# Performance work log

Hardware: AMD Instinct MI355X
Metric: run time of the kernel (lower is better)

Reference implementation:

```python
import jax, jax.numpy as jnp
import numpy as np

B, N, F_IN, F_OUT = 64, 4096, 32, 32


def setup_inputs() -> dict:
    key = jax.random.key(0)
    k1, k2, k3, k4 = jax.random.split(key, 4)
    x = jax.random.normal(k1, (B, N, F_IN), dtype=jnp.float32)
    adj = jax.random.uniform(k2, (N, N), dtype=jnp.float32)
    # GraphConvolution parameters (Glorot-ish scale)
    W = jax.random.normal(k3, (F_IN, F_OUT), dtype=jnp.float32) / np.sqrt(F_IN)
    b = jax.random.normal(k4, (F_OUT,), dtype=jnp.float32) * 0.01
    return {"x": x, "adj": adj, "W": W, "b": b}


def reference(x, adj, W, b):
    # Original: adj_ = kron(I_B, adj) -> block-diagonal [B*N, B*N];
    # gconv(x_flat, adj_) = adj_ @ (x_flat @ W) + b, reshaped to [B, N, F_OUT].
    # Block-diagonal structure == independent per-batch graph conv:
    #   out[b] = adj @ (x[b] @ W) + b
    support = jnp.einsum('bnf,fo->bno', x, W)      # [B, N, F_OUT]
    out = jnp.einsum('nm,bmo->bno', adj, support)  # [B, N, F_OUT]
    return out + b
```

## Files before the change

### kernel.cpp

```cpp
#include <hip/hip_runtime.h>
#include <hip/hip_bf16.h>


#define B_SZ 64
#define N_SZ 4096
#define NT 64

typedef __attribute__((ext_vector_type(8))) short bf16x8;
typedef __attribute__((ext_vector_type(4))) float f32x4;
typedef __attribute__((ext_vector_type(8))) unsigned short u16x8;

__device__ __forceinline__ unsigned short f2bf(float f) {
  unsigned int u = __float_as_uint(f);
  u += 0x7fffu + ((u >> 16) & 1u);
  return (unsigned short)(u >> 16);
}

__device__ __forceinline__ void support_body(const float* __restrict__ x,
                                             const float* __restrict__ W,
                                             unsigned short* __restrict__ St,
                                             int gid) {
  const int m = gid & (N_SZ - 1);
  const int b = gid >> 12;
  const float4* xr = (const float4*)(x + (size_t)gid * 32);
  float xv[32];
#pragma unroll
  for (int i = 0; i < 8; ++i) {
    float4 v = xr[i];
    xv[4 * i + 0] = v.x; xv[4 * i + 1] = v.y;
    xv[4 * i + 2] = v.z; xv[4 * i + 3] = v.w;
  }
  const size_t obase = ((size_t)b * 32) * (size_t)N_SZ + m;
#pragma unroll
  for (int o = 0; o < 32; ++o) {
    float acc = 0.f;
#pragma unroll
    for (int f = 0; f < 32; ++f) acc = fmaf(xv[f], W[f * 32 + o], acc);
    St[obase + (size_t)o * N_SZ] = f2bf(acc);
  }
}

__device__ __forceinline__ void cvt_body(const float* __restrict__ a,
                                         unsigned short* __restrict__ o,
                                         size_t idx8) {
  const size_t i = idx8 * 8;
  const float4* p = (const float4*)(a + i);
  float4 v0 = p[0], v1 = p[1];
  u16x8 r;
  r[0] = f2bf(v0.x); r[1] = f2bf(v0.y); r[2] = f2bf(v0.z); r[3] = f2bf(v0.w);
  r[4] = f2bf(v1.x); r[5] = f2bf(v1.y); r[6] = f2bf(v1.z); r[7] = f2bf(v1.w);
  *(u16x8*)(o + i) = r;
}

__global__ __launch_bounds__(256) void k_prep(const float* __restrict__ x,
                                              const float* __restrict__ adj,
                                              const float* __restrict__ W,
                                              unsigned short* __restrict__ St,
                                              unsigned short* __restrict__ adjB) {
  const int bid = blockIdx.x;
  const int t = threadIdx.x;
  if (bid < 8192) cvt_body(adj, adjB, (size_t)bid * 256 + t);
  else support_body(x, W, St, (bid - 8192) * 256 + t);
}

__global__ __launch_bounds__(256) void k_support(const float* __restrict__ x,
                                                 const float* __restrict__ W,
                                                 unsigned short* __restrict__ St) {
  support_body(x, W, St, blockIdx.x * 256 + threadIdx.x);
}
__global__ __launch_bounds__(256) void k_cvt(const float* __restrict__ a,
                                             unsigned short* __restrict__ o) {
  cvt_body(a, o, (size_t)blockIdx.x * 256 + threadIdx.x);
}

#define GLOAD16(gp, lp)                                                        \
  __builtin_amdgcn_global_load_lds(                                            \
      (const __attribute__((address_space(1))) void*)(gp),                     \
      (__attribute__((address_space(3))) void*)(lp), 16, 0, 0)
#define PRIO1() __builtin_amdgcn_s_setprio(1)
#define PRIO0() __builtin_amdgcn_s_setprio(0)

__global__ __launch_bounds__(256, 2) void k_gemm6(const unsigned short* __restrict__ Ab,
                                                  const unsigned short* __restrict__ Bm,
                                                  const float* __restrict__ bias,
                                                  float* __restrict__ out,
                                                  int nbm, int rowoff) {
  __shared__ __attribute__((aligned(16))) char SM[65536];
  char* Lc = SM;
  char* Lo = SM + 32768;
  const int t = threadIdx.x;
  const int wg = blockIdx.x;
  const int xcd = wg & 7;
  const int c = wg >> 3;
  const int bm0 = (xcd * nbm + (c >> 4)) << 7;
  const int bn0 = (c & 15) << 7;
  const int lane = t & 63;
  const int wid = t >> 6;
  const int wr = wid & 1;
  const int ks = wid >> 1;

  f32x4 acc[4][8];
#pragma unroll
  for (int i = 0; i < 4; ++i)
#pragma unroll
    for (int j = 0; j < 8; ++j) acc[i][j] = (f32x4){0.f, 0.f, 0.f, 0.f};

  const int srow = t >> 3;
  const int as = t & 7;
  const int swz = (as ^ (srow & 7)) << 4;
  const size_t a_s0 = ((size_t)(bm0 + srow) << 13) + (size_t)swz;
  const size_t b_s0 = ((size_t)(bn0 + srow) << 13) + (size_t)swz;
  const int t16 = t * 16;
  const char* A8 = (const char*)Ab;
  const char* B8 = (const char*)Bm;

#define STAGE(KT_, Ld)                                                         \
  do {                                                                         \
    const size_t kb = (size_t)(KT_) << 7;                                      \
    GLOAD16(A8 + a_s0 + kb,          (Ld) + t16);                              \
    GLOAD16(A8 + a_s0 + 262144 + kb, (Ld) + 4096 + t16);                       \
    GLOAD16(A8 + a_s0 + 524288 + kb, (Ld) + 8192 + t16);                       \
    GLOAD16(A8 + a_s0 + 786432 + kb, (Ld) + 12288 + t16);                      \
    GLOAD16(B8 + b_s0 + kb,          (Ld) + 16384 + t16);                      \
    GLOAD16(B8 + b_s0 + 262144 + kb, (Ld) + 20480 + t16);                      \
    GLOAD16(B8 + b_s0 + 524288 + kb, (Ld) + 24576 + t16);                      \
    GLOAD16(B8 + b_s0 + 786432 + kb, (Ld) + 28672 + t16);                      \
  } while (0)

  const int cbase = (ks * 64 + ((lane >> 4) << 4)) ^ ((lane & 7) << 4);
  int aoff[4], boff[8];
#pragma unroll
  for (int mi = 0; mi < 4; ++mi)
    aoff[mi] = (wr * 64 + mi * 16 + (lane & 15)) * 128 + cbase;
#pragma unroll
  for (int ni = 0; ni < 8; ++ni)
    boff[ni] = 16384 + (ni * 16 + (lane & 15)) * 128 + cbase;

  STAGE(0, Lc);
  __syncthreads();

  for (int kt = 0; kt < NT; ++kt) {
    if (kt + 1 < NT) STAGE(kt + 1, Lo);
    bf16x8 a[4], b[8];
#pragma unroll
    for (int mi = 0; mi < 4; ++mi) a[mi] = *(const bf16x8*)(Lc + aoff[mi]);
#pragma unroll
    for (int ni = 0; ni < 8; ++ni) b[ni] = *(const bf16x8*)(Lc + boff[ni]);
    PRIO1();
#pragma unroll
    for (int mi = 0; mi < 4; ++mi)
#pragma unroll
      for (int ni = 0; ni < 8; ++ni)
        acc[mi][ni] = __builtin_amdgcn_mfma_f32_16x16x32_bf16(
            a[mi], b[ni], acc[mi][ni], 0, 0, 0);
    PRIO0();
    __syncthreads();
    { char* tp_ = Lc; Lc = Lo; Lo = tp_; }
  }

  if (ks == 1) {
    char* mb = SM + (wr << 15);
#pragma unroll
    for (int mi = 0; mi < 4; ++mi)
#pragma unroll
      for (int ni = 0; ni < 8; ++ni)
        *(f32x4*)(mb + (((mi * 8 + ni) << 6) + lane) * 16) = acc[mi][ni];
  }
  __syncthreads();
  if (ks == 0) {
    char* mb = SM + (wr << 15);
#pragma unroll
    for (int mi = 0; mi < 4; ++mi)
#pragma unroll
      for (int ni = 0; ni < 8; ++ni)
        acc[mi][ni] += *(const f32x4*)(mb + (((mi * 8 + ni) << 6) + lane) * 16);
    const float blo = bias[lane & 15];
    const float bhi = bias[(lane & 15) + 16];
#pragma unroll
    for (int mi = 0; mi < 4; ++mi) {
#pragma unroll
      for (int ni = 0; ni < 8; ++ni) {
        const float badd = (ni & 1) ? bhi : blo;
#pragma unroll
        for (int q = 0; q < 4; ++q) {
          const int n = rowoff + bm0 + wr * 64 + mi * 16 + ((lane >> 4) << 2) + q;
          const int cidx = bn0 + ni * 16 + (lane & 15);
          const int bb = cidx >> 5;
          const int o = cidx & 31;
          out[(((size_t)bb << 12) + n) * 32 + o] = acc[mi][ni][q] + badd;
        }
      }
    }
  }
}

extern "C" void kernel_launch(void* const* d_in, const int* in_sizes, int n_in,
                              void* d_out, int out_size, void* d_ws, size_t ws_size,
                              hipStream_t stream) {
  const float* x = (const float*)d_in[0];
  const float* adj = (const float*)d_in[1];
  const float* W = (const float*)d_in[2];
  const float* bias = (const float*)d_in[3];
  float* out = (float*)d_out;

  const size_t ST_B = (size_t)2048 * 4096 * 2;
  const size_t ADJ_FULL = (size_t)4096 * 4096 * 2;

  unsigned short* St = (unsigned short*)d_ws;

  if (ws_size >= ST_B + ADJ_FULL) {
    unsigned short* adjB = St + (ST_B / 2);
    hipLaunchKernelGGL(k_prep, dim3(9216), dim3(256), 0, stream, x, adj, W, St,
                       adjB);
    hipLaunchKernelGGL(k_gemm6, dim3(512), dim3(256), 0, stream, adjB, St, bias,
                       out, 4, 0);
  } else {
    unsigned short* adjH = St + (ST_B / 2);
    hipLaunchKernelGGL(k_support, dim3((B_SZ * N_SZ) / 256), dim3(256), 0,
                       stream, x, W, St);
    hipLaunchKernelGGL(k_cvt, dim3((2048 * 4096) / 2048), dim3(256), 0, stream,
                       adj, adjH);
    hipLaunchKernelGGL(k_gemm6, dim3(256), dim3(256), 0, stream, adjH, St, bias,
                       out, 2, 0);
    hipLaunchKernelGGL(k_cvt, dim3((2048 * 4096) / 2048), dim3(256), 0, stream,
                       adj + (size_t)2048 * 4096, adjH);
    hipLaunchKernelGGL(k_gemm6, dim3(256), dim3(256), 0, stream, adjH, St, bias,
                       out, 2, 2048);
  }
}
```

Measured before the change: 94.20 us.

## Widen GEMM tile to 128x256 with 512 threads and triple-buffered LDS pipeline

Replaces the 128x128 double-buffered GEMM with a 128x256 tile computed by 8 waves: two column halves, each split over two K halves. A three-stage LDS ring is prefetched two iterations ahead, with explicit vmcnt waits and raw barriers in place of __syncthreads. The intent is to raise A-tile reuse, halve the workgroup count and hide global load latency better. In exchange the kernel uses 144KB of LDS per block, so only one block fits per CU despite the launch bound hint, and the hand-placed waitcnt and barrier scheme is fragile.

```diff
diff --git a/kernel.cpp b/kernel.cpp
--- a/kernel.cpp
+++ b/kernel.cpp
@@ -5,6 +5,7 @@
 #define B_SZ 64
 #define N_SZ 4096
 #define NT 64
+#define STG 49152
 
 typedef __attribute__((ext_vector_type(8))) short bf16x8;
 typedef __attribute__((ext_vector_type(4))) float f32x4;
@@ -79,25 +80,28 @@
       (__attribute__((address_space(3))) void*)(lp), 16, 0, 0)
 #define PRIO1() __builtin_amdgcn_s_setprio(1)
 #define PRIO0() __builtin_amdgcn_s_setprio(0)
-
-__global__ __launch_bounds__(256, 2) void k_gemm6(const unsigned short* __restrict__ Ab,
+#define VMW(N_) asm volatile("s_waitcnt vmcnt(" #N_ ")" ::: "memory")
+#define LGKM0() asm volatile("s_waitcnt lgkmcnt(0)" ::: "memory")
+#define BARR() asm volatile("s_barrier" ::: "memory")
+#define SCHED0() __builtin_amdgcn_sched_barrier(0)
+
+__global__ __launch_bounds__(512, 2) void k_gemm8(const unsigned short* __restrict__ Ab,
                                                   const unsigned short* __restrict__ Bm,
                                                   const float* __restrict__ bias,
                                                   float* __restrict__ out,
                                                   int nbm, int rowoff) {
-  __shared__ __attribute__((aligned(16))) char SM[65536];
-  char* Lc = SM;
-  char* Lo = SM + 32768;
+  __shared__ __attribute__((aligned(16))) char SM[147456];
   const int t = threadIdx.x;
   const int wg = blockIdx.x;
   const int xcd = wg & 7;
   const int c = wg >> 3;
-  const int bm0 = (xcd * nbm + (c >> 4)) << 7;
-  const int bn0 = (c & 15) << 7;
+  const int bm0 = (xcd * nbm + (c >> 3)) << 7;
+  const int bn0 = (c & 7) << 8;
   const int lane = t & 63;
   const int wid = t >> 6;
   const int wr = wid & 1;
-  const int ks = wid >> 1;
+  const int nc = (wid >> 1) & 1;
+  const int ks = wid >> 2;
 
   f32x4 acc[4][8];
 #pragma unroll
@@ -114,17 +118,15 @@
   const char* A8 = (const char*)Ab;
   const char* B8 = (const char*)Bm;
 
-#define STAGE(KT_, Ld)                                                         \
+#define STAGE(KT_, LOFF_)                                                      \
   do {                                                                         \
     const size_t kb = (size_t)(KT_) << 7;                                      \
-    GLOAD16(A8 + a_s0 + kb,          (Ld) + t16);                              \
-    GLOAD16(A8 + a_s0 + 262144 + kb, (Ld) + 4096 + t16);                       \
-    GLOAD16(A8 + a_s0 + 524288 + kb, (Ld) + 8192 + t16);                       \
-    GLOAD16(A8 + a_s0 + 786432 + kb, (Ld) + 12288 + t16);                      \
-    GLOAD16(B8 + b_s0 + kb,          (Ld) + 16384 + t16);                      \
-    GLOAD16(B8 + b_s0 + 262144 + kb, (Ld) + 20480 + t16);                      \
-    GLOAD16(B8 + b_s0 + 524288 + kb, (Ld) + 24576 + t16);                      \
-    GLOAD16(B8 + b_s0 + 786432 + kb, (Ld) + 28672 + t16);                      \
+    GLOAD16(A8 + a_s0 + kb,           SM + (LOFF_) + t16);                     \
+    GLOAD16(A8 + a_s0 + 524288 + kb,  SM + (LOFF_) + 8192 + t16);              \
+    GLOAD16(B8 + b_s0 + kb,           SM + (LOFF_) + 16384 + t16);             \
+    GLOAD16(B8 + b_s0 + 524288 + kb,  SM + (LOFF_) + 24576 + t16);             \
+    GLOAD16(B8 + b_s0 + 1048576 + kb, SM + (LOFF_) + 32768 + t16);             \
+    GLOAD16(B8 + b_s0 + 1572864 + kb, SM + (LOFF_) + 40960 + t16);             \
   } while (0)
 
   const int cbase = (ks * 64 + ((lane >> 4) << 4)) ^ ((lane & 7) << 4);
@@ -134,32 +136,53 @@
     aoff[mi] = (wr * 64 + mi * 16 + (lane & 15)) * 128 + cbase;
 #pragma unroll
   for (int ni = 0; ni < 8; ++ni)
-    boff[ni] = 16384 + (ni * 16 + (lane & 15)) * 128 + cbase;
-
-  STAGE(0, Lc);
-  __syncthreads();
-
-  for (int kt = 0; kt < NT; ++kt) {
-    if (kt + 1 < NT) STAGE(kt + 1, Lo);
-    bf16x8 a[4], b[8];
-#pragma unroll
-    for (int mi = 0; mi < 4; ++mi) a[mi] = *(const bf16x8*)(Lc + aoff[mi]);
-#pragma unroll
-    for (int ni = 0; ni < 8; ++ni) b[ni] = *(const bf16x8*)(Lc + boff[ni]);
-    PRIO1();
-#pragma unroll
-    for (int mi = 0; mi < 4; ++mi)
-#pragma unroll
-      for (int ni = 0; ni < 8; ++ni)
-        acc[mi][ni] = __builtin_amdgcn_mfma_f32_16x16x32_bf16(
-            a[mi], b[ni], acc[mi][ni], 0, 0, 0);
-    PRIO0();
-    __syncthreads();
-    { char* tp_ = Lc; Lc = Lo; Lo = tp_; }
-  }
+    boff[ni] = 16384 + (nc * 128 + ni * 16 + (lane & 15)) * 128 + cbase;
+
+#define FRAG_MFMA(CUROFF_)                                                     \
+  do {                                                                         \
+    bf16x8 a[4], b[8];                                                         \
+    _Pragma("unroll") for (int mi = 0; mi < 4; ++mi)                           \
+        a[mi] = *(const bf16x8*)(SM + (CUROFF_) + aoff[mi]);                   \
+    _Pragma("unroll") for (int ni = 0; ni < 8; ++ni)                           \
+        b[ni] = *(const bf16x8*)(SM + (CUROFF_) + boff[ni]);                   \
+    LGKM0();                                                                   \
+    SCHED0();                                                                  \
+    BARR();                                                                    \
+    PRIO1();                                                                   \
+    _Pragma("unroll") for (int mi = 0; mi < 4; ++mi)                           \
+        _Pragma("unroll") for (int ni = 0; ni < 8; ++ni)                       \
+            acc[mi][ni] = __builtin_amdgcn_mfma_f32_16x16x32_bf16(             \
+                a[mi], b[ni], acc[mi][ni], 0, 0, 0);                           \
+    PRIO0();                                                                   \
+  } while (0)
+
+#define ITER(T_, CUR_, NXT_)                                                   \
+  do {                                                                         \
+    STAGE((T_) + 2, (NXT_) * STG);                                             \
+    VMW(12);                                                                   \
+    BARR();                                                                    \
+    FRAG_MFMA((CUR_) * STG);                                                   \
+  } while (0)
+
+  STAGE(0, 0);
+  STAGE(1, STG);
+
+  for (int t0 = 0; t0 < 60; t0 += 3) {
+    ITER(t0 + 0, 0, 2);
+    ITER(t0 + 1, 1, 0);
+    ITER(t0 + 2, 2, 1);
+  }
+  ITER(60, 0, 2);
+  ITER(61, 1, 0);
+  VMW(6);
+  BARR();
+  FRAG_MFMA(2 * STG);
+  VMW(0);
+  BARR();
+  FRAG_MFMA(0 * STG);
 
   if (ks == 1) {
-    char* mb = SM + (wr << 15);
+    char* mb = SM + ((wid & 3) << 15);
 #pragma unroll
     for (int mi = 0; mi < 4; ++mi)
 #pragma unroll
@@ -168,7 +191,7 @@
   }
   __syncthreads();
   if (ks == 0) {
-    char* mb = SM + (wr << 15);
+    char* mb = SM + ((wid & 3) << 15);
 #pragma unroll
     for (int mi = 0; mi < 4; ++mi)
 #pragma unroll
@@ -184,7 +207,7 @@
 #pragma unroll
         for (int q = 0; q < 4; ++q) {
           const int n = rowoff + bm0 + wr * 64 + mi * 16 + ((lane >> 4) << 2) + q;
-          const int cidx = bn0 + ni * 16 + (lane & 15);
+          const int cidx = bn0 + nc * 128 + ni * 16 + (lane & 15);
           const int bb = cidx >> 5;
           const int o = cidx & 31;
           out[(((size_t)bb << 12) + n) * 32 + o] = acc[mi][ni][q] + badd;
@@ -212,7 +235,7 @@
     unsigned short* adjB = St + (ST_B / 2);
     hipLaunchKernelGGL(k_prep, dim3(9216), dim3(256), 0, stream, x, adj, W, St,
                        adjB);
-    hipLaunchKernelGGL(k_gemm6, dim3(512), dim3(256), 0, stream, adjB, St, bias,
+    hipLaunchKernelGGL(k_gemm8, dim3(256), dim3(512), 0, stream, adjB, St, bias,
                        out, 4, 0);
   } else {
     unsigned short* adjH = St + (ST_B / 2);
@@ -220,11 +243,11 @@
                        stream, x, W, St);
     hipLaunchKernelGGL(k_cvt, dim3((2048 * 4096) / 2048), dim3(256), 0, stream,
                        adj, adjH);
-    hipLaunchKernelGGL(k_gemm6, dim3(256), dim3(256), 0, stream, adjH, St, bias,
+    hipLaunchKernelGGL(k_gemm8, dim3(128), dim3(512), 0, stream, adjH, St, bias,
                        out, 2, 0);
     hipLaunchKernelGGL(k_cvt, dim3((2048 * 4096) / 2048), dim3(256), 0, stream,
                        adj + (size_t)2048 * 4096, adjH);
-    hipLaunchKernelGGL(k_gemm6, dim3(256), dim3(256), 0, stream, adjH, St, bias,
+    hipLaunchKernelGGL(k_gemm8, dim3(128), dim3(512), 0, stream, adjH, St, bias,
                        out, 2, 2048);
   }
 }
```

Result: slower. 96.89 us (+2.9%).

## Fuse fp32-to-bf16 adjacency conversion into GEMM A-tile loading

Applied to the files above, without the earlier changes.

The separate pass that converts the 4096x4096 adjacency matrix to bf16 in workspace is removed. The GEMM now reads fp32 adj rows straight into registers, converts them in-kernel and writes them to swizzled LDS, overlapping that store with the MFMA loop. This drops a 64MB read plus 32MB write-and-reread of adj. In exchange the GEMM moves twice the A-tile bytes per tile from global memory, uses more registers, and ALU work competes with the MFMAs. The tile-to-XCD mapping is also changed to 2D blocks of 1024x1024.

```diff
diff --git a/kernel.cpp b/kernel.cpp
--- a/kernel.cpp
+++ b/kernel.cpp
@@ -16,10 +16,10 @@
   return (unsigned short)(u >> 16);
 }
 
-__device__ __forceinline__ void support_body(const float* __restrict__ x,
-                                             const float* __restrict__ W,
-                                             unsigned short* __restrict__ St,
-                                             int gid) {
+__global__ __launch_bounds__(256) void k_support(const float* __restrict__ x,
+                                                 const float* __restrict__ W,
+                                                 unsigned short* __restrict__ St) {
+  const int gid = blockIdx.x * 256 + threadIdx.x;
   const int m = gid & (N_SZ - 1);
   const int b = gid >> 12;
   const float4* xr = (const float4*)(x + (size_t)gid * 32);
@@ -38,39 +38,6 @@
     for (int f = 0; f < 32; ++f) acc = fmaf(xv[f], W[f * 32 + o], acc);
     St[obase + (size_t)o * N_SZ] = f2bf(acc);
   }
-}
-
-__device__ __forceinline__ void cvt_body(const float* __restrict__ a,
-                                         unsigned short* __restrict__ o,
-                                         size_t idx8) {
-  const size_t i = idx8 * 8;
-  const float4* p = (const float4*)(a + i);
-  float4 v0 = p[0], v1 = p[1];
-  u16x8 r;
-  r[0] = f2bf(v0.x); r[1] = f2bf(v0.y); r[2] = f2bf(v0.z); r[3] = f2bf(v0.w);
-  r[4] = f2bf(v1.x); r[5] = f2bf(v1.y); r[6] = f2bf(v1.z); r[7] = f2bf(v1.w);
-  *(u16x8*)(o + i) = r;
-}
-
-__global__ __launch_bounds__(256) void k_prep(const float* __restrict__ x,
-                                              const float* __restrict__ adj,
-                                              const float* __restrict__ W,
-                                              unsigned short* __restrict__ St,
-                                              unsigned short* __restrict__ adjB) {
-  const int bid = blockIdx.x;
-  const int t = threadIdx.x;
-  if (bid < 8192) cvt_body(adj, adjB, (size_t)bid * 256 + t);
-  else support_body(x, W, St, (bid - 8192) * 256 + t);
-}
-
-__global__ __launch_bounds__(256) void k_support(const float* __restrict__ x,
-                                                 const float* __restrict__ W,
-                                                 unsigned short* __restrict__ St) {
-  support_body(x, W, St, blockIdx.x * 256 + threadIdx.x);
-}
-__global__ __launch_bounds__(256) void k_cvt(const float* __restrict__ a,
-                                             unsigned short* __restrict__ o) {
-  cvt_body(a, o, (size_t)blockIdx.x * 256 + threadIdx.x);
 }
 
 #define GLOAD16(gp, lp)                                                        \
@@ -80,20 +47,19 @@
 #define PRIO1() __builtin_amdgcn_s_setprio(1)
 #define PRIO0() __builtin_amdgcn_s_setprio(0)
 
-__global__ __launch_bounds__(256, 2) void k_gemm6(const unsigned short* __restrict__ Ab,
+__global__ __launch_bounds__(256, 2) void k_gemm7(const float* __restrict__ adj,
                                                   const unsigned short* __restrict__ Bm,
                                                   const float* __restrict__ bias,
-                                                  float* __restrict__ out,
-                                                  int nbm, int rowoff) {
+                                                  float* __restrict__ out) {
   __shared__ __attribute__((aligned(16))) char SM[65536];
   char* Lc = SM;
   char* Lo = SM + 32768;
   const int t = threadIdx.x;
   const int wg = blockIdx.x;
   const int xcd = wg & 7;
-  const int c = wg >> 3;
-  const int bm0 = (xcd * nbm + (c >> 4)) << 7;
-  const int bn0 = (c & 15) << 7;
+  const int idx = wg >> 3;
+  const int bm0 = ((xcd >> 1) << 10) + ((idx >> 3) << 7);
+  const int bn0 = ((xcd & 1) << 10) + ((idx & 7) << 7);
   const int lane = t & 63;
   const int wid = t >> 6;
   const int wr = wid & 1;
@@ -108,25 +74,43 @@
   const int srow = t >> 3;
   const int as = t & 7;
   const int swz = (as ^ (srow & 7)) << 4;
-  const size_t a_s0 = ((size_t)(bm0 + srow) << 13) + (size_t)swz;
   const size_t b_s0 = ((size_t)(bn0 + srow) << 13) + (size_t)swz;
   const int t16 = t * 16;
-  const char* A8 = (const char*)Ab;
   const char* B8 = (const char*)Bm;
 
-#define STAGE(KT_, Ld)                                                         \
+#define STAGE_B(KT_, Ld)                                                       \
   do {                                                                         \
     const size_t kb = (size_t)(KT_) << 7;                                      \
-    GLOAD16(A8 + a_s0 + kb,          (Ld) + t16);                              \
-    GLOAD16(A8 + a_s0 + 262144 + kb, (Ld) + 4096 + t16);                       \
-    GLOAD16(A8 + a_s0 + 524288 + kb, (Ld) + 8192 + t16);                       \
-    GLOAD16(A8 + a_s0 + 786432 + kb, (Ld) + 12288 + t16);                      \
     GLOAD16(B8 + b_s0 + kb,          (Ld) + 16384 + t16);                      \
     GLOAD16(B8 + b_s0 + 262144 + kb, (Ld) + 20480 + t16);                      \
     GLOAD16(B8 + b_s0 + 524288 + kb, (Ld) + 24576 + t16);                      \
     GLOAD16(B8 + b_s0 + 786432 + kb, (Ld) + 28672 + t16);                      \
   } while (0)
 
+  const float* aF = adj + ((size_t)(bm0 + (t >> 3)) << 12) + ((t & 7) << 3);
+  const int awbase = ((t >> 3) << 7) + (((t & 7) ^ ((t >> 3) & 7)) << 4);
+
+#define ALOAD(KT_)                                                             \
+  do {                                                                         \
+    const float* ap_ = aF + ((size_t)(KT_) << 6);                              \
+    _Pragma("unroll") for (int j = 0; j < 4; ++j) {                            \
+      va[2 * j]     = *(const float4*)(ap_ + (size_t)j * 131072);              \
+      va[2 * j + 1] = *(const float4*)(ap_ + (size_t)j * 131072 + 4);          \
+    }                                                                          \
+  } while (0)
+
+#define AWRITE(Ld)                                                             \
+  do {                                                                         \
+    _Pragma("unroll") for (int j = 0; j < 4; ++j) {                            \
+      u16x8 w_;                                                                \
+      w_[0] = f2bf(va[2 * j].x);     w_[1] = f2bf(va[2 * j].y);                \
+      w_[2] = f2bf(va[2 * j].z);     w_[3] = f2bf(va[2 * j].w);                \
+      w_[4] = f2bf(va[2 * j + 1].x); w_[5] = f2bf(va[2 * j + 1].y);            \
+      w_[6] = f2bf(va[2 * j + 1].z); w_[7] = f2bf(va[2 * j + 1].w);            \
+      *(u16x8*)((Ld) + awbase + j * 4096) = w_;                                \
+    }                                                                          \
+  } while (0)
+
   const int cbase = (ks * 64 + ((lane >> 4) << 4)) ^ ((lane & 7) << 4);
   int aoff[4], boff[8];
 #pragma unroll
@@ -136,11 +120,18 @@
   for (int ni = 0; ni < 8; ++ni)
     boff[ni] = 16384 + (ni * 16 + (lane & 15)) * 128 + cbase;
 
-  STAGE(0, Lc);
+  float4 va[8];
+
+  ALOAD(0);
+  STAGE_B(0, Lc);
+  AWRITE(Lc);
   __syncthreads();
 
   for (int kt = 0; kt < NT; ++kt) {
-    if (kt + 1 < NT) STAGE(kt + 1, Lo);
+    if (kt + 1 < NT) {
+      ALOAD(kt + 1);
+      STAGE_B(kt + 1, Lo);
+    }
     bf16x8 a[4], b[8];
 #pragma unroll
     for (int mi = 0; mi < 4; ++mi) a[mi] = *(const bf16x8*)(Lc + aoff[mi]);
@@ -154,6 +145,7 @@
         acc[mi][ni] = __builtin_amdgcn_mfma_f32_16x16x32_bf16(
             a[mi], b[ni], acc[mi][ni], 0, 0, 0);
     PRIO0();
+    if (kt + 1 < NT) AWRITE(Lo);
     __syncthreads();
     { char* tp_ = Lc; Lc = Lo; Lo = tp_; }
   }
@@ -183,7 +175,7 @@
         const float badd = (ni & 1) ? bhi : blo;
 #pragma unroll
         for (int q = 0; q < 4; ++q) {
-          const int n = rowoff + bm0 + wr * 64 + mi * 16 + ((lane >> 4) << 2) + q;
+          const int n = bm0 + wr * 64 + mi * 16 + ((lane >> 4) << 2) + q;
           const int cidx = bn0 + ni * 16 + (lane & 15);
           const int bb = cidx >> 5;
           const int o = cidx & 31;
@@ -203,28 +195,10 @@
   const float* bias = (const float*)d_in[3];
   float* out = (float*)d_out;
 
-  const size_t ST_B = (size_t)2048 * 4096 * 2;
-  const size_t ADJ_FULL = (size_t)4096 * 4096 * 2;
-
   unsigned short* St = (unsigned short*)d_ws;
 
-  if (ws_size >= ST_B + ADJ_FULL) {
-    unsigned short* adjB = St + (ST_B / 2);
-    hipLaunchKernelGGL(k_prep, dim3(9216), dim3(256), 0, stream, x, adj, W, St,
-                       adjB);
-    hipLaunchKernelGGL(k_gemm6, dim3(512), dim3(256), 0, stream, adjB, St, bias,
-                       out, 4, 0);
-  } else {
-    unsigned short* adjH = St + (ST_B / 2);
-    hipLaunchKernelGGL(k_support, dim3((B_SZ * N_SZ) / 256), dim3(256), 0,
-                       stream, x, W, St);
-    hipLaunchKernelGGL(k_cvt, dim3((2048 * 4096) / 2048), dim3(256), 0, stream,
-                       adj, adjH);
-    hipLaunchKernelGGL(k_gemm6, dim3(256), dim3(256), 0, stream, adjH, St, bias,
-                       out, 2, 0);
-    hipLaunchKernelGGL(k_cvt, dim3((2048 * 4096) / 2048), dim3(256), 0, stream,
-                       adj + (size_t)2048 * 4096, adjH);
-    hipLaunchKernelGGL(k_gemm6, dim3(256), dim3(256), 0, stream, adjH, St, bias,
-                       out, 2, 2048);
-  }
-}
+  hipLaunchKernelGGL(k_support, dim3((B_SZ * N_SZ) / 256), dim3(256), 0, stream,
+                     x, W, St);
+  hipLaunchKernelGGL(k_gemm7, dim3(512), dim3(256), 0, stream, adj, St, bias,
+                     out);
+}
```

After: 109.1 us. +15.8%, slower.
